# Optimization experiments

Hardware: AMD Instinct MI355X
Metric: run time of the kernel (lower is better)

## Reference

```python
import jax, jax.numpy as jnp
import numpy as np


def fwht(x):
    """Unnormalized fast Walsh-Hadamard transform over a 1-D vector (len = power of 2).
    Matches the torch chunk/cat stage ordering (MSB-first butterfly)."""
    n = x.shape[0]
    ll = int(round(np.log2(n)))
    for ii in range(ll):
        x = x.reshape(2 ** ii, 2, -1)
        x = jnp.concatenate([x[:, :1] + x[:, 1:], x[:, :1] - x[:, 1:]], axis=1)
    return x.reshape(n)


@jax.custom_vjp
def fwht_ff(x):
    # mirrors torch FastWalshHadamard.apply: plain FWHT forward,
    # backward = FWHT(grad) / sqrt(n) (as defined in the original autograd Function)
    return fwht(x)

def _fwht_ff_fwd(x):
    scale = jnp.asarray(1.0 / np.sqrt(float(x.shape[0])), x.dtype)
    return fwht(x), scale

def _fwht_ff_bwd(scale, g):
    return (scale * fwht(g),)

fwht_ff.defvjp(_fwht_ff_fwd, _fwht_ff_bwd)


def fastfood(theta, BB, Pi, GG, DD):
    """Fastfood projection of theta (dim dd) to DD dims using fixed vars."""
    LL = BB.shape[0]
    dd = theta.shape[0]
    k = min(dd, LL)  # F.pad with negative pad truncates; replicate that
    xx = jnp.zeros(LL, theta.dtype).at[:k].set(theta[:k])
    m2 = fwht(BB * xx)          # H B x
    m4 = m2[Pi] * GG            # G Pi H B x
    m5 = fwht_ff(m4)            # H G Pi H B x
    divisor = jnp.sqrt(LL * jnp.sum(GG * GG))
    return m5[:DD] / (divisor * np.sqrt(float(DD) / LL))


def _mk_ff_vars(key, DD):
    ll = int(np.ceil(np.log2(DD)))
    LL = 2 ** ll
    k1, k2, k3 = jax.random.split(key, 3)
    BB = jax.random.randint(k1, (LL,), 0, 2).astype(jnp.float32) * 2.0 - 1.0
    Pi = jax.random.permutation(k2, LL).astype(jnp.int32)
    GG = jax.random.normal(k3, (LL,), dtype=jnp.float32)
    return BB, Pi, GG


D_IN, D_HID, D_OUT = 768, 3072, 768
INTRINSIC = 2048
BATCH = 256


def setup_inputs() -> dict:
    key = jax.random.key(0)
    ks = jax.random.split(key, 12)
    x = jax.random.normal(ks[0], (BATCH, D_IN), dtype=jnp.float32)
    # original initializes intrinsic_parameter to zeros; use small randn so the
    # Fastfood path contributes non-trivially to the output for testing
    theta = jax.random.normal(ks[1], (INTRINSIC,), dtype=jnp.float32) * 0.01
    init_W1 = jax.random.normal(ks[2], (D_HID, D_IN), dtype=jnp.float32) * 0.02
    init_b1 = jax.random.normal(ks[3], (D_HID,), dtype=jnp.float32) * 0.02
    init_W2 = jax.random.normal(ks[4], (D_OUT, D_HID), dtype=jnp.float32) * 0.02
    init_b2 = jax.random.normal(ks[5], (D_OUT,), dtype=jnp.float32) * 0.02
    BB_W1, Pi_W1, GG_W1 = _mk_ff_vars(ks[6], D_HID * D_IN)
    BB_b1, Pi_b1, GG_b1 = _mk_ff_vars(ks[7], D_HID)
    BB_W2, Pi_W2, GG_W2 = _mk_ff_vars(ks[8], D_OUT * D_HID)
    BB_b2, Pi_b2, GG_b2 = _mk_ff_vars(ks[9], D_OUT)
    return {
        'x': x, 'theta': theta,
        'init_W1': init_W1, 'init_b1': init_b1, 'init_W2': init_W2, 'init_b2': init_b2,
        'BB_W1': BB_W1, 'Pi_W1': Pi_W1, 'GG_W1': GG_W1,
        'BB_b1': BB_b1, 'Pi_b1': Pi_b1, 'GG_b1': GG_b1,
        'BB_W2': BB_W2, 'Pi_W2': Pi_W2, 'GG_W2': GG_W2,
        'BB_b2': BB_b2, 'Pi_b2': Pi_b2, 'GG_b2': GG_b2,
    }


def reference(x, theta, init_W1, init_b1, init_W2, init_b2,
              BB_W1, Pi_W1, GG_W1, BB_b1, Pi_b1, GG_b1,
              BB_W2, Pi_W2, GG_W2, BB_b2, Pi_b2, GG_b2):
    # param = initial_value + fastfood(theta) for every wrapped parameter
    W1 = init_W1 + fastfood(theta, BB_W1, Pi_W1, GG_W1, init_W1.size).reshape(init_W1.shape)
    b1 = init_b1 + fastfood(theta, BB_b1, Pi_b1, GG_b1, init_b1.size)
    W2 = init_W2 + fastfood(theta, BB_W2, Pi_W2, GG_W2, init_W2.size).reshape(init_W2.shape)
    b2 = init_b2 + fastfood(theta, BB_b2, Pi_b2, GG_b2, init_b2.size)
    # wrapped module forward: Linear -> ReLU -> Linear
    h = jax.nn.relu(x @ W1.T + b1)
    return h @ W2.T + b2
```

## Files before the change

### kernel.cpp

```cpp
#include <hip/hip_runtime.h>
#include <hip/hip_bf16.h>

typedef __attribute__((ext_vector_type(8))) short bf16x8;
typedef __attribute__((ext_vector_type(8))) unsigned short u16x8;
typedef __attribute__((ext_vector_type(4))) float f32x4;

template <int N, int S>
__device__ __forceinline__ void reg_fwht(float* v) {
#pragma unroll
  for (int h = 1; h < N; h <<= 1)
#pragma unroll
    for (int g = 0; g < N; g += 2 * h)
#pragma unroll
      for (int j = 0; j < h; ++j) {
        float a = v[(g + j) * S], b = v[(g + j + h) * S];
        v[(g + j) * S] = a + b;
        v[(g + j + h) * S] = a - b;
      }
}

__device__ __forceinline__ unsigned short f2bf(float f) {
  unsigned u = __float_as_uint(f);
  unsigned r = (u + 0x7fff + ((u >> 16) & 1)) >> 16;
  return (unsigned short)r;
}

__device__ __forceinline__ void lds_fwht(float* s, int n, int tid, int T) {
  for (int h = 1; h < n; h <<= 1) {
    __syncthreads();
    for (int t = tid; t < (n >> 1); t += T) {
      int i0 = ((t & ~(h - 1)) << 1) | (t & (h - 1));
      int i1 = i0 + h;
      float a = s[i0], b = s[i1];
      s[i0] = a + b;
      s[i1] = a - b;
    }
  }
  __syncthreads();
}

__device__ __forceinline__ void fwht2048_block(float w[8], float* pad,
                                               float* dst, int t) {
  reg_fwht<8, 1>(w);
#pragma unroll
  for (int j = 0; j < 8; ++j) {
    int i = t + 256 * j;
    pad[i + 4 * (i >> 5)] = w[j];
  }
  __syncthreads();
  {
    int base = 8 * t + 4 * (t >> 2);
    float4 a = *(float4*)(pad + base);
    float4 b = *(float4*)(pad + base + 4);
    float u[8] = {a.x, a.y, a.z, a.w, b.x, b.y, b.z, b.w};
    reg_fwht<8, 1>(u);
    *(float4*)(pad + base) = make_float4(u[0], u[1], u[2], u[3]);
    *(float4*)(pad + base + 4) = make_float4(u[4], u[5], u[6], u[7]);
  }
  __syncthreads();
  {
    int b0 = (t & 7) + 64 * (t >> 3);
    float u[8];
#pragma unroll
    for (int j = 0; j < 8; ++j) {
      int i = b0 + 8 * j;
      u[j] = pad[i + 4 * (i >> 5)];
    }
    reg_fwht<8, 1>(u);
#pragma unroll
    for (int j = 0; j < 8; ++j) {
      int i = b0 + 8 * j;
      pad[i + 4 * (i >> 5)] = u[j];
    }
  }
  __syncthreads();
#pragma unroll
  for (int g = 0; g < 2; ++g) {
    int b0 = (t & 63) + 256 * ((g << 2) | (t >> 6));
    float u[4];
#pragma unroll
    for (int j = 0; j < 4; ++j) {
      int i = b0 + 64 * j;
      u[j] = pad[i + 4 * (i >> 5)];
    }
    reg_fwht<4, 1>(u);
#pragma unroll
    for (int j = 0; j < 4; ++j) dst[b0 + 64 * j] = u[j];
  }
  __syncthreads();
}

#define LLW 4194304

__global__ __launch_bounds__(256) void k_front(
    const float* __restrict__ BB1, const int* __restrict__ Pi1,
    const float* __restrict__ GG1, const float* __restrict__ BB2,
    const int* __restrict__ Pi2, const float* __restrict__ GG2,
    unsigned short* __restrict__ m4b, float* __restrict__ partial,
    const float* __restrict__ theta, const float* __restrict__ BBb1,
    const int* __restrict__ Pib1, const float* __restrict__ GGb1,
    const float* __restrict__ ib1, float* __restrict__ b1w,
    const float* __restrict__ BBb2, const int* __restrict__ Pib2,
    const float* __restrict__ GGb2, const float* __restrict__ ib2,
    float* __restrict__ b2w, const float* __restrict__ x,
    __hip_bfloat16* __restrict__ xb) {
  __shared__ __align__(16) float s[9216];
  __shared__ float red[4];
  int b = blockIdx.x, t = threadIdx.x;

  if (b < 1024) {
    int pipe = b >> 9, chunk = b & 511;
    const float* BB = pipe ? BB2 : BB1;
    const int* Pi = pipe ? Pi2 : Pi1;
    const float* GG = pipe ? GG2 : GG1;

    {
      float w8[8];
#pragma unroll
      for (int j = 0; j < 8; ++j) {
        int i = t + 256 * j;
        w8[j] = BB[i] * theta[i];
      }
      fwht2048_block(w8, s + 2304, s, t);
    }

    long base = (long)chunk * 8192;
    const int4* p4 = (const int4*)(Pi + base);
    const float4* g4 = (const float4*)(GG + base);
    float v[32];
    float lsum = 0.f;
#pragma unroll
    for (int j = 0; j < 8; ++j) {
      int4 p = p4[t + j * 256];
      float4 g = g4[t + j * 256];
      lsum += g.x * g.x + g.y * g.y + g.z * g.z + g.w * g.w;
      v[j * 4 + 0] = s[p.x & 2047] * g.x;
      v[j * 4 + 1] = s[p.y & 2047] * g.y;
      v[j * 4 + 2] = s[p.z & 2047] * g.z;
      v[j * 4 + 3] = s[p.w & 2047] * g.w;
    }
    for (int off = 32; off; off >>= 1) lsum += __shfl_down(lsum, off, 64);
    if ((t & 63) == 0) red[t >> 6] = lsum;

#pragma unroll
    for (int e = 0; e < 4; ++e) reg_fwht<8, 4>(v + e);

    __syncthreads();
    if (t == 0) partial[pipe * 512 + chunk] = red[0] + red[1] + red[2] + red[3];

#pragma unroll
    for (int j = 0; j < 8; ++j) {
      int A = t * 4 + 4 * (t >> 3) + j * 1152;
      *(float4*)(s + A) =
          make_float4(v[j * 4], v[j * 4 + 1], v[j * 4 + 2], v[j * 4 + 3]);
    }
    __syncthreads();
    {
      int b0 = (t & 31) + (t >> 5) * 1024;
      float w[32];
#pragma unroll
      for (int j2 = 0; j2 < 32; ++j2) {
        int i = b0 + j2 * 32;
        w[j2] = s[i + 4 * (i >> 5)];
      }
      reg_fwht<32, 1>(w);
#pragma unroll
      for (int j2 = 0; j2 < 32; ++j2) {
        int i = b0 + j2 * 32;
        s[i + 4 * (i >> 5)] = w[j2];
      }
    }
    __syncthreads();
#pragma unroll
    for (int q = 0; q < 8; ++q) {
      float4 r = *(const float4*)(s + t * 36 + q * 4);
      v[q * 4 + 0] = r.x;
      v[q * 4 + 1] = r.y;
      v[q * 4 + 2] = r.z;
      v[q * 4 + 3] = r.w;
    }
    reg_fwht<32, 1>(v);
    unsigned short* o = m4b + (long)pipe * LLW;
    long a0 = (long)(2 * t) * 8192 + (long)chunk * 16;
#pragma unroll
    for (int q = 0; q < 4; ++q) {
      u16x8 pk;
#pragma unroll
      for (int e = 0; e < 8; ++e) pk[e] = f2bf(v[q * 8 + e]);
      *(u16x8*)(o + a0 + (q >> 1) * 8192 + (q & 1) * 8) = pk;
    }
  } else if (b == 1024) {
    float* tabd = s + 6144;
    float w[8];
#pragma unroll
    for (int j = 0; j < 8; ++j) {
      int i = t + 256 * j;
      w[j] = BBb1[i] * theta[i];
    }
    fwht2048_block(w, s, tabd, t);

    float w16[16];
    float lsum = 0.f;
#pragma unroll
    for (int j = 0; j < 16; ++j) {
      int i = t + 256 * j;
      float g = GGb1[i];
      lsum += g * g;
      w16[j] = tabd[Pib1[i] & 2047] * g;
    }
    reg_fwht<16, 1>(w16);
#pragma unroll
    for (int j = 0; j < 16; ++j) {
      int i = t + 256 * j;
      s[i + 4 * (i >> 5)] = w16[j];
    }
    for (int off = 32; off; off >>= 1) lsum += __shfl_down(lsum, off, 64);
    if ((t & 63) == 0) s[4608 + (t >> 6)] = lsum;
    __syncthreads();
    float S = s[4608] + s[4609] + s[4610] + s[4611];
    {
      int base16 = 16 * t + 4 * (t >> 1);
      float u[16];
#pragma unroll
      for (int q = 0; q < 4; ++q) {
        float4 r = *(float4*)(s + base16 + q * 4);
        u[q * 4 + 0] = r.x;
        u[q * 4 + 1] = r.y;
        u[q * 4 + 2] = r.z;
        u[q * 4 + 3] = r.w;
      }
      reg_fwht<16, 1>(u);
#pragma unroll
      for (int q = 0; q < 4; ++q)
        *(float4*)(s + base16 + q * 4) =
            make_float4(u[q * 4], u[q * 4 + 1], u[q * 4 + 2], u[q * 4 + 3]);
    }
    __syncthreads();
    {
      float scale = 1.0f / sqrtf(S * 3072.0f);
      int b0 = (t & 15) + 256 * (t >> 4);
      float u[16];
#pragma unroll
      for (int j = 0; j < 16; ++j) {
        int i = b0 + 16 * j;
        u[j] = s[i + 4 * (i >> 5)];
      }
      reg_fwht<16, 1>(u);
#pragma unroll
      for (int j = 0; j < 16; ++j) {
        int i = b0 + 16 * j;
        if (i < 3072) b1w[i] = ib1[i] + u[j] * scale;
      }
    }
  } else if (b == 1025) {
    float* tab2 = s;
    float* m42 = s + 1024;
    for (int i = t; i < 1024; i += 256) tab2[i] = BBb2[i] * theta[i];
    lds_fwht(tab2, 1024, t, 256);
    float lsum = 0.f;
    for (int i = t; i < 1024; i += 256) {
      float g = GGb2[i];
      lsum += g * g;
      m42[i] = tab2[Pib2[i] & 1023] * g;
    }
    for (int off = 32; off; off >>= 1) lsum += __shfl_down(lsum, off, 64);
    if ((t & 63) == 0) s[2048 + (t >> 6)] = lsum;
    lds_fwht(m42, 1024, t, 256);
    float S = s[2048] + s[2049] + s[2050] + s[2051];
    float scale = 1.0f / sqrtf(S * 768.0f);
    for (int i = t; i < 768; i += 256) b2w[i] = ib2[i] + m42[i] * scale;
  } else {
    int id0 = (b - 1026) * 256 + t;
#pragma unroll
    for (int it = 0; it < 2; ++it) {
      int id = id0 + it * 24576;
      float4 xv = ((const float4*)x)[id];
      ushort4 o;
      o.x = f2bf(xv.x);
      o.y = f2bf(xv.y);
      o.z = f2bf(xv.z);
      o.w = f2bf(xv.w);
      ((ushort4*)xb)[id] = o;
    }
  }
}

__device__ __forceinline__ void f2c_body(const unsigned short* __restrict__ mpipe,
                                         const float* __restrict__ initW,
                                         unsigned short* __restrict__ outW,
                                         const float* __restrict__ partial_p,
                                         int lb, int t, float* s, float* red) {
  int g = ((lb & 7) << 6) | (lb >> 3);
  int l0 = g * 16;
  const unsigned short* mp = mpipe + (long)g * 8192;

  {
    float ps = partial_p[t] + partial_p[256 + t];
    for (int off = 32; off; off >>= 1) ps += __shfl_down(ps, off, 64);
    if ((t & 63) == 0) red[t >> 6] = ps;
  }

#pragma unroll
  for (int q = 0; q < 4; ++q) {
    u16x8 raw = *(const u16x8*)(mp + t * 32 + q * 8);
    int r = 2 * t + (q >> 1), cb = (q & 1) * 8;
    float* dp = s + r * 20 + (r >> 5) * 16 + cb;
    float4 f0, f1v;
    f0.x = __uint_as_float((unsigned)raw[0] << 16);
    f0.y = __uint_as_float((unsigned)raw[1] << 16);
    f0.z = __uint_as_float((unsigned)raw[2] << 16);
    f0.w = __uint_as_float((unsigned)raw[3] << 16);
    f1v.x = __uint_as_float((unsigned)raw[4] << 16);
    f1v.y = __uint_as_float((unsigned)raw[5] << 16);
    f1v.z = __uint_as_float((unsigned)raw[6] << 16);
    f1v.w = __uint_as_float((unsigned)raw[7] << 16);
    *(float4*)dp = f0;
    *(float4*)(dp + 4) = f1v;
  }
  __syncthreads();

  {
    int c = t & 15, rg = t >> 4;
    float w[32];
#pragma unroll
    for (int j = 0; j < 32; ++j) {
      int r = rg * 32 + j;
      w[j] = s[r * 20 + (r >> 5) * 16 + c];
    }
    reg_fwht<32, 1>(w);
#pragma unroll
    for (int j = 0; j < 32; ++j) {
      int r = rg * 32 + j;
      s[r * 20 + (r >> 5) * 16 + c] = w[j];
    }
  }
  __syncthreads();

  {
    int c = t & 15;
    float w[32];
#pragma unroll
    for (int k = 0; k < 2; ++k) {
      int b0 = (t >> 4) * 2 + k;
#pragma unroll
      for (int j4 = 0; j4 < 16; ++j4) {
        int r = b0 + 32 * j4;
        w[k * 16 + j4] = s[r * 20 + (r >> 5) * 16 + c];
      }
      reg_fwht<16, 1>(w + k * 16);
#pragma unroll
      for (int j4 = 0; j4 < 16; ++j4) {
        int r = b0 + 32 * j4;
        s[r * 20 + (r >> 5) * 16 + c] = w[k * 16 + j4];
      }
    }
  }
  __syncthreads();

  float S = red[0] + red[1] + red[2] + red[3];
  float scale = 1.0f / sqrtf(S * 2359296.0f);
#pragma unroll
  for (int u = 0; u < 5; ++u) {
    int idx = t + u * 256;
    if (idx < 1152) {
      int r = idx >> 2, c4 = (idx & 3) * 4;
      const float* sp = s + r * 20 + (r >> 5) * 16 + c4;
      long gi = (long)r * 8192 + l0 + c4;
      float4 iv = *(const float4*)(initW + gi);
      ushort4 pk;
      pk.x = f2bf(iv.x + sp[0] * scale);
      pk.y = f2bf(iv.y + sp[1] * scale);
      pk.z = f2bf(iv.z + sp[2] * scale);
      pk.w = f2bf(iv.w + sp[3] * scale);
      *(ushort4*)(outW + gi) = pk;
    }
  }
}

template <int NACC, int SPLITK, bool RELU, bool OUT_BF16>
__device__ __forceinline__ void gemm_body(
    const __hip_bfloat16* __restrict__ A, const __hip_bfloat16* __restrict__ B,
    const float* __restrict__ bias, void* __restrict__ C, int M, int N, int K,
    int bid, int tid, float* red) {
  int wave = tid >> 6, lane = tid & 63;
  int tileid = bid * (4 / SPLITK) + wave / SPLITK;
  int sk = wave % SPLITK;
  int ntiles = N / (16 * NACC);
  int mt = tileid / ntiles, nt = tileid % ntiles;
  int ml = lane & 15;
  int q = lane >> 4;
  const short* As = (const short*)A;
  const short* Bs = (const short*)B;
  long arow = (long)(mt * 16 + ml) * K + q * 8;
  int KS = K / SPLITK, k0 = sk * KS;
  f32x4 acc[NACC] = {};
  for (int k = k0; k < k0 + KS; k += 32) {
    bf16x8 av = *(const bf16x8*)(As + arow + k);
#pragma unroll
    for (int a = 0; a < NACC; ++a) {
      int n = nt * 16 * NACC + a * 16 + ml;
      bf16x8 bv = *(const bf16x8*)(Bs + (long)n * K + q * 8 + k);
      acc[a] = __builtin_amdgcn_mfma_f32_16x16x32_bf16(av, bv, acc[a], 0, 0, 0);
    }
  }
#pragma unroll
  for (int a = 0; a < NACC; ++a)
#pragma unroll
    for (int r = 0; r < 4; ++r)
      red[(wave * NACC + a) * 320 + lane * 5 + r] = acc[a][r];
  __syncthreads();
  if (sk == 0) {
#pragma unroll
    for (int a = 0; a < NACC; ++a) {
      int n = nt * 16 * NACC + a * 16 + ml;
      float bv = bias[n];
#pragma unroll
      for (int r = 0; r < 4; ++r) {
        float vv = bv;
#pragma unroll
        for (int j = 0; j < SPLITK; ++j)
          vv += red[((wave + j) * NACC + a) * 320 + lane * 5 + r];
        int mm = mt * 16 + q * 4 + r;
        if (RELU) vv = fmaxf(vv, 0.f);
        if (OUT_BF16)
          ((__hip_bfloat16*)C)[(long)mm * N + n] = __float2bfloat16(vv);
        else
          ((float*)C)[(long)mm * N + n] = vv;
      }
    }
  }
}

__global__ __launch_bounds__(256) void k_f2c_a(
    const unsigned short* __restrict__ m4b, const float* __restrict__ iW1,
    const float* __restrict__ partial, __hip_bfloat16* __restrict__ W1b) {
  __shared__ __align__(16) float s[10480];
  __shared__ float red[4];
  f2c_body(m4b, iW1, (unsigned short*)W1b, partial, blockIdx.x, threadIdx.x, s,
           red);
}

__global__ __launch_bounds__(256) void k_mix(
    const unsigned short* __restrict__ m4b, const float* __restrict__ iW2,
    const float* __restrict__ partial, __hip_bfloat16* __restrict__ W2b,
    const __hip_bfloat16* __restrict__ xb, const __hip_bfloat16* __restrict__ W1b,
    const float* __restrict__ b1w, __hip_bfloat16* __restrict__ hb) {
  __shared__ __align__(16) float s[10480];
  __shared__ float red[4];
  int b = blockIdx.x, t = threadIdx.x;
  if (b < 512) {
    f2c_body(m4b + (long)LLW, iW2, (unsigned short*)W2b, partial + 512, b, t,
             s, red);
  } else {
    gemm_body<2, 2, true, true>(xb, W1b, b1w, hb, 256, 3072, 768, b - 512, t,
                                s);
  }
}

template <int NACC, int SPLITK, bool RELU, bool OUT_BF16>
__global__ __launch_bounds__(256) void k_gemm(
    const __hip_bfloat16* __restrict__ A, const __hip_bfloat16* __restrict__ B,
    const float* __restrict__ bias, void* __restrict__ C, int M, int N, int K) {
  __shared__ float red[4 * NACC * 320];
  gemm_body<NACC, SPLITK, RELU, OUT_BF16>(A, B, bias, C, M, N, K, blockIdx.x,
                                          threadIdx.x, red);
}

#define OFF_PART 0
#define OFF_M2S 4096
#define OFF_M4B (OFF_M2S + 16384)
#define OFF_W1B (OFF_M4B + 2 * LLW * 2)
#define OFF_W2B (OFF_W1B + 4718592)
#define OFF_HB (OFF_W2B + 4718592)
#define OFF_XB (OFF_HB + 1572864)
#define OFF_B1 (OFF_XB + 393216)
#define OFF_B2 (OFF_B1 + 12288)

extern "C" void kernel_launch(void* const* d_in, const int* in_sizes, int n_in,
                              void* d_out, int out_size, void* d_ws,
                              size_t ws_size, hipStream_t stream) {
  const float* x = (const float*)d_in[0];
  const float* theta = (const float*)d_in[1];
  const float* iW1 = (const float*)d_in[2];
  const float* ib1 = (const float*)d_in[3];
  const float* iW2 = (const float*)d_in[4];
  const float* ib2 = (const float*)d_in[5];
  const float* BB_W1 = (const float*)d_in[6];
  const int* Pi_W1 = (const int*)d_in[7];
  const float* GG_W1 = (const float*)d_in[8];
  const float* BB_b1 = (const float*)d_in[9];
  const int* Pi_b1 = (const int*)d_in[10];
  const float* GG_b1 = (const float*)d_in[11];
  const float* BB_W2 = (const float*)d_in[12];
  const int* Pi_W2 = (const int*)d_in[13];
  const float* GG_W2 = (const float*)d_in[14];
  const float* BB_b2 = (const float*)d_in[15];
  const int* Pi_b2 = (const int*)d_in[16];
  const float* GG_b2 = (const float*)d_in[17];

  char* ws = (char*)d_ws;
  float* partial = (float*)(ws + OFF_PART);
  unsigned short* m4b = (unsigned short*)(ws + OFF_M4B);
  __hip_bfloat16* W1b = (__hip_bfloat16*)(ws + OFF_W1B);
  __hip_bfloat16* W2b = (__hip_bfloat16*)(ws + OFF_W2B);
  __hip_bfloat16* hb = (__hip_bfloat16*)(ws + OFF_HB);
  __hip_bfloat16* xb = (__hip_bfloat16*)(ws + OFF_XB);
  float* b1w = (float*)(ws + OFF_B1);
  float* b2w = (float*)(ws + OFF_B2);

  k_front<<<1122, 256, 0, stream>>>(BB_W1, Pi_W1, GG_W1, BB_W2, Pi_W2, GG_W2,
                                    m4b, partial, theta, BB_b1, Pi_b1, GG_b1,
                                    ib1, b1w, BB_b2, Pi_b2, GG_b2, ib2, b2w, x,
                                    xb);
  k_f2c_a<<<512, 256, 0, stream>>>(m4b, iW1, partial, W1b);
  k_mix<<<1280, 256, 0, stream>>>(m4b, iW2, partial, W2b, xb, W1b, b1w, hb);
  k_gemm<1, 4, false, false><<<768, 256, 0, stream>>>(hb, W2b, b2w, d_out, 256,
                                                      768, 3072);
}
```

Measured before the change: 218.1 us.

## Fuse all stages into one cooperative persistent kernel with grid syncs

Replaces the four separate launches with a single cooperative kernel of 1024 blocks that runs the front FWHT, the second FWHT/convert stage, GEMM1 and GEMM2, separated by grid-wide barriers. The small bias jobs and the x-to-bf16 conversion are folded into the front-stage blocks. The LDS padding in f2c is also removed so the kernel fits at four blocks per CU, and GEMM1 now uses three accumulators with 4-way split-K to cover 1024 blocks. The goal is to cut launch gaps and kernel tails, at the cost of grid-sync overhead and more bank conflicts from the unpadded LDS layout. If the cooperative launch fails, separate kernels run as a fallback.

```diff
diff --git a/kernel.cpp b/kernel.cpp
--- a/kernel.cpp
+++ b/kernel.cpp
@@ -1,9 +1,28 @@
 #include <hip/hip_runtime.h>
 #include <hip/hip_bf16.h>
+#include <hip/hip_cooperative_groups.h>
+
+namespace cg = cooperative_groups;
 
 typedef __attribute__((ext_vector_type(8))) short bf16x8;
 typedef __attribute__((ext_vector_type(8))) unsigned short u16x8;
 typedef __attribute__((ext_vector_type(4))) float f32x4;
+
+#define LLW 4194304
+
+struct FFParams {
+  const float* BB1; const int* Pi1; const float* GG1;
+  const float* BB2; const int* Pi2; const float* GG2;
+  unsigned short* m4b; float* partial; const float* theta;
+  const float* BBb1; const int* Pib1; const float* GGb1; const float* ib1;
+  float* b1w;
+  const float* BBb2; const int* Pib2; const float* GGb2; const float* ib2;
+  float* b2w;
+  const float* x; __hip_bfloat16* xb;
+  const float* iW1; const float* iW2;
+  __hip_bfloat16* W1b; __hip_bfloat16* W2b;
+  __hip_bfloat16* hb; float* out;
+};
 
 template <int N, int S>
 __device__ __forceinline__ void reg_fwht(float* v) {
@@ -90,206 +109,179 @@
   __syncthreads();
 }
 
-#define LLW 4194304
-
-__global__ __launch_bounds__(256) void k_front(
-    const float* __restrict__ BB1, const int* __restrict__ Pi1,
-    const float* __restrict__ GG1, const float* __restrict__ BB2,
-    const int* __restrict__ Pi2, const float* __restrict__ GG2,
-    unsigned short* __restrict__ m4b, float* __restrict__ partial,
-    const float* __restrict__ theta, const float* __restrict__ BBb1,
-    const int* __restrict__ Pib1, const float* __restrict__ GGb1,
-    const float* __restrict__ ib1, float* __restrict__ b1w,
-    const float* __restrict__ BBb2, const int* __restrict__ Pib2,
-    const float* __restrict__ GGb2, const float* __restrict__ ib2,
-    float* __restrict__ b2w, const float* __restrict__ x,
-    __hip_bfloat16* __restrict__ xb) {
-  __shared__ __align__(16) float s[9216];
-  __shared__ float red[4];
-  int b = blockIdx.x, t = threadIdx.x;
-
-  if (b < 1024) {
-    int pipe = b >> 9, chunk = b & 511;
-    const float* BB = pipe ? BB2 : BB1;
-    const int* Pi = pipe ? Pi2 : Pi1;
-    const float* GG = pipe ? GG2 : GG1;
-
-    {
-      float w8[8];
-#pragma unroll
-      for (int j = 0; j < 8; ++j) {
-        int i = t + 256 * j;
-        w8[j] = BB[i] * theta[i];
-      }
-      fwht2048_block(w8, s + 2304, s, t);
-    }
-
-    long base = (long)chunk * 8192;
-    const int4* p4 = (const int4*)(Pi + base);
-    const float4* g4 = (const float4*)(GG + base);
-    float v[32];
-    float lsum = 0.f;
-#pragma unroll
-    for (int j = 0; j < 8; ++j) {
-      int4 p = p4[t + j * 256];
-      float4 g = g4[t + j * 256];
-      lsum += g.x * g.x + g.y * g.y + g.z * g.z + g.w * g.w;
-      v[j * 4 + 0] = s[p.x & 2047] * g.x;
-      v[j * 4 + 1] = s[p.y & 2047] * g.y;
-      v[j * 4 + 2] = s[p.z & 2047] * g.z;
-      v[j * 4 + 3] = s[p.w & 2047] * g.w;
-    }
-    for (int off = 32; off; off >>= 1) lsum += __shfl_down(lsum, off, 64);
-    if ((t & 63) == 0) red[t >> 6] = lsum;
-
-#pragma unroll
-    for (int e = 0; e < 4; ++e) reg_fwht<8, 4>(v + e);
-
-    __syncthreads();
-    if (t == 0) partial[pipe * 512 + chunk] = red[0] + red[1] + red[2] + red[3];
-
-#pragma unroll
-    for (int j = 0; j < 8; ++j) {
-      int A = t * 4 + 4 * (t >> 3) + j * 1152;
-      *(float4*)(s + A) =
-          make_float4(v[j * 4], v[j * 4 + 1], v[j * 4 + 2], v[j * 4 + 3]);
-    }
-    __syncthreads();
-    {
-      int b0 = (t & 31) + (t >> 5) * 1024;
-      float w[32];
-#pragma unroll
-      for (int j2 = 0; j2 < 32; ++j2) {
-        int i = b0 + j2 * 32;
-        w[j2] = s[i + 4 * (i >> 5)];
-      }
-      reg_fwht<32, 1>(w);
-#pragma unroll
-      for (int j2 = 0; j2 < 32; ++j2) {
-        int i = b0 + j2 * 32;
-        s[i + 4 * (i >> 5)] = w[j2];
-      }
-    }
-    __syncthreads();
-#pragma unroll
-    for (int q = 0; q < 8; ++q) {
-      float4 r = *(const float4*)(s + t * 36 + q * 4);
-      v[q * 4 + 0] = r.x;
-      v[q * 4 + 1] = r.y;
-      v[q * 4 + 2] = r.z;
-      v[q * 4 + 3] = r.w;
-    }
-    reg_fwht<32, 1>(v);
-    unsigned short* o = m4b + (long)pipe * LLW;
-    long a0 = (long)(2 * t) * 8192 + (long)chunk * 16;
-#pragma unroll
-    for (int q = 0; q < 4; ++q) {
-      u16x8 pk;
-#pragma unroll
-      for (int e = 0; e < 8; ++e) pk[e] = f2bf(v[q * 8 + e]);
-      *(u16x8*)(o + a0 + (q >> 1) * 8192 + (q & 1) * 8) = pk;
-    }
-  } else if (b == 1024) {
-    float* tabd = s + 6144;
-    float w[8];
+__device__ __forceinline__ void front_pipe(const FFParams& p, int b, int t,
+                                           float* s, float* red) {
+  int pipe = b >> 9, chunk = b & 511;
+  const float* BB = pipe ? p.BB2 : p.BB1;
+  const int* Pi = pipe ? p.Pi2 : p.Pi1;
+  const float* GG = pipe ? p.GG2 : p.GG1;
+
+  {
+    float w8[8];
 #pragma unroll
     for (int j = 0; j < 8; ++j) {
       int i = t + 256 * j;
-      w[j] = BBb1[i] * theta[i];
-    }
-    fwht2048_block(w, s, tabd, t);
-
-    float w16[16];
-    float lsum = 0.f;
+      w8[j] = BB[i] * p.theta[i];
+    }
+    fwht2048_block(w8, s + 2304, s, t);
+  }
+
+  long base = (long)chunk * 8192;
+  const int4* p4 = (const int4*)(Pi + base);
+  const float4* g4 = (const float4*)(GG + base);
+  float v[32];
+  float lsum = 0.f;
+#pragma unroll
+  for (int j = 0; j < 8; ++j) {
+    int4 pp = p4[t + j * 256];
+    float4 g = g4[t + j * 256];
+    lsum += g.x * g.x + g.y * g.y + g.z * g.z + g.w * g.w;
+    v[j * 4 + 0] = s[pp.x & 2047] * g.x;
+    v[j * 4 + 1] = s[pp.y & 2047] * g.y;
+    v[j * 4 + 2] = s[pp.z & 2047] * g.z;
+    v[j * 4 + 3] = s[pp.w & 2047] * g.w;
+  }
+  for (int off = 32; off; off >>= 1) lsum += __shfl_down(lsum, off, 64);
+  if ((t & 63) == 0) red[t >> 6] = lsum;
+
+#pragma unroll
+  for (int e = 0; e < 4; ++e) reg_fwht<8, 4>(v + e);
+
+  __syncthreads();
+  if (t == 0)
+    p.partial[pipe * 512 + chunk] = red[0] + red[1] + red[2] + red[3];
+
+#pragma unroll
+  for (int j = 0; j < 8; ++j) {
+    int A = t * 4 + 4 * (t >> 3) + j * 1152;
+    *(float4*)(s + A) =
+        make_float4(v[j * 4], v[j * 4 + 1], v[j * 4 + 2], v[j * 4 + 3]);
+  }
+  __syncthreads();
+  {
+    int b0 = (t & 31) + (t >> 5) * 1024;
+    float w[32];
+#pragma unroll
+    for (int j2 = 0; j2 < 32; ++j2) {
+      int i = b0 + j2 * 32;
+      w[j2] = s[i + 4 * (i >> 5)];
+    }
+    reg_fwht<32, 1>(w);
+#pragma unroll
+    for (int j2 = 0; j2 < 32; ++j2) {
+      int i = b0 + j2 * 32;
+      s[i + 4 * (i >> 5)] = w[j2];
+    }
+  }
+  __syncthreads();
+#pragma unroll
+  for (int q = 0; q < 8; ++q) {
+    float4 r = *(const float4*)(s + t * 36 + q * 4);
+    v[q * 4 + 0] = r.x;
+    v[q * 4 + 1] = r.y;
+    v[q * 4 + 2] = r.z;
+    v[q * 4 + 3] = r.w;
+  }
+  reg_fwht<32, 1>(v);
+  unsigned short* o = p.m4b + (long)pipe * LLW;
+  long a0 = (long)(2 * t) * 8192 + (long)chunk * 16;
+#pragma unroll
+  for (int q = 0; q < 4; ++q) {
+    u16x8 pk;
+#pragma unroll
+    for (int e = 0; e < 8; ++e) pk[e] = f2bf(v[q * 8 + e]);
+    *(u16x8*)(o + a0 + (q >> 1) * 8192 + (q & 1) * 8) = pk;
+  }
+}
+
+__device__ __forceinline__ void bias1_job(const FFParams& p, int t, float* s) {
+  float* tabd = s + 6144;
+  float w[8];
+#pragma unroll
+  for (int j = 0; j < 8; ++j) {
+    int i = t + 256 * j;
+    w[j] = p.BBb1[i] * p.theta[i];
+  }
+  fwht2048_block(w, s, tabd, t);
+
+  float w16[16];
+  float lsum = 0.f;
+#pragma unroll
+  for (int j = 0; j < 16; ++j) {
+    int i = t + 256 * j;
+    float g = p.GGb1[i];
+    lsum += g * g;
+    w16[j] = tabd[p.Pib1[i] & 2047] * g;
+  }
+  reg_fwht<16, 1>(w16);
+#pragma unroll
+  for (int j = 0; j < 16; ++j) {
+    int i = t + 256 * j;
+    s[i + 4 * (i >> 5)] = w16[j];
+  }
+  for (int off = 32; off; off >>= 1) lsum += __shfl_down(lsum, off, 64);
+  if ((t & 63) == 0) s[4608 + (t >> 6)] = lsum;
+  __syncthreads();
+  float S = s[4608] + s[4609] + s[4610] + s[4611];
+  {
+    int base16 = 16 * t + 4 * (t >> 1);
+    float u[16];
+#pragma unroll
+    for (int q = 0; q < 4; ++q) {
+      float4 r = *(float4*)(s + base16 + q * 4);
+      u[q * 4 + 0] = r.x;
+      u[q * 4 + 1] = r.y;
+      u[q * 4 + 2] = r.z;
+      u[q * 4 + 3] = r.w;
+    }
+    reg_fwht<16, 1>(u);
+#pragma unroll
+    for (int q = 0; q < 4; ++q)
+      *(float4*)(s + base16 + q * 4) =
+          make_float4(u[q * 4], u[q * 4 + 1], u[q * 4 + 2], u[q * 4 + 3]);
+  }
+  __syncthreads();
+  {
+    float scale = 1.0f / sqrtf(S * 3072.0f);
+    int b0 = (t & 15) + 256 * (t >> 4);
+    float u[16];
 #pragma unroll
     for (int j = 0; j < 16; ++j) {
-      int i = t + 256 * j;
-      float g = GGb1[i];
-      lsum += g * g;
-      w16[j] = tabd[Pib1[i] & 2047] * g;
-    }
-    reg_fwht<16, 1>(w16);
+      int i = b0 + 16 * j;
+      u[j] = s[i + 4 * (i >> 5)];
+    }
+    reg_fwht<16, 1>(u);
 #pragma unroll
     for (int j = 0; j < 16; ++j) {
-      int i = t + 256 * j;
-      s[i + 4 * (i >> 5)] = w16[j];
-    }
-    for (int off = 32; off; off >>= 1) lsum += __shfl_down(lsum, off, 64);
-    if ((t & 63) == 0) s[4608 + (t >> 6)] = lsum;
-    __syncthreads();
-    float S = s[4608] + s[4609] + s[4610] + s[4611];
-    {
-      int base16 = 16 * t + 4 * (t >> 1);
-      float u[16];
-#pragma unroll
-      for (int q = 0; q < 4; ++q) {
-        float4 r = *(float4*)(s + base16 + q * 4);
-        u[q * 4 + 0] = r.x;
-        u[q * 4 + 1] = r.y;
-        u[q * 4 + 2] = r.z;
-        u[q * 4 + 3] = r.w;
-      }
-      reg_fwht<16, 1>(u);
-#pragma unroll
-      for (int q = 0; q < 4; ++q)
-        *(float4*)(s + base16 + q * 4) =
-            make_float4(u[q * 4], u[q * 4 + 1], u[q * 4 + 2], u[q * 4 + 3]);
-    }
-    __syncthreads();
-    {
-      float scale = 1.0f / sqrtf(S * 3072.0f);
-      int b0 = (t & 15) + 256 * (t >> 4);
-      float u[16];
-#pragma unroll
-      for (int j = 0; j < 16; ++j) {
-        int i = b0 + 16 * j;
-        u[j] = s[i + 4 * (i >> 5)];
-      }
-      reg_fwht<16, 1>(u);
-#pragma unroll
-      for (int j = 0; j < 16; ++j) {
-        int i = b0 + 16 * j;
-        if (i < 3072) b1w[i] = ib1[i] + u[j] * scale;
-      }
-    }
-  } else if (b == 1025) {
-    float* tab2 = s;
-    float* m42 = s + 1024;
-    for (int i = t; i < 1024; i += 256) tab2[i] = BBb2[i] * theta[i];
-    lds_fwht(tab2, 1024, t, 256);
-    float lsum = 0.f;
-    for (int i = t; i < 1024; i += 256) {
-      float g = GGb2[i];
-      lsum += g * g;
-      m42[i] = tab2[Pib2[i] & 1023] * g;
-    }
-    for (int off = 32; off; off >>= 1) lsum += __shfl_down(lsum, off, 64);
-    if ((t & 63) == 0) s[2048 + (t >> 6)] = lsum;
-    lds_fwht(m42, 1024, t, 256);
-    float S = s[2048] + s[2049] + s[2050] + s[2051];
-    float scale = 1.0f / sqrtf(S * 768.0f);
-    for (int i = t; i < 768; i += 256) b2w[i] = ib2[i] + m42[i] * scale;
-  } else {
-    int id0 = (b - 1026) * 256 + t;
-#pragma unroll
-    for (int it = 0; it < 2; ++it) {
-      int id = id0 + it * 24576;
-      float4 xv = ((const float4*)x)[id];
-      ushort4 o;
-      o.x = f2bf(xv.x);
-      o.y = f2bf(xv.y);
-      o.z = f2bf(xv.z);
-      o.w = f2bf(xv.w);
-      ((ushort4*)xb)[id] = o;
-    }
-  }
-}
-
-__device__ __forceinline__ void f2c_body(const unsigned short* __restrict__ mpipe,
-                                         const float* __restrict__ initW,
-                                         unsigned short* __restrict__ outW,
-                                         const float* __restrict__ partial_p,
-                                         int lb, int t, float* s, float* red) {
+      int i = b0 + 16 * j;
+      if (i < 3072) p.b1w[i] = p.ib1[i] + u[j] * scale;
+    }
+  }
+}
+
+__device__ __forceinline__ void bias2_job(const FFParams& p, int t, float* s) {
+  float* tab2 = s;
+  float* m42 = s + 1024;
+  for (int i = t; i < 1024; i += 256) tab2[i] = p.BBb2[i] * p.theta[i];
+  lds_fwht(tab2, 1024, t, 256);
+  float lsum = 0.f;
+  for (int i = t; i < 1024; i += 256) {
+    float g = p.GGb2[i];
+    lsum += g * g;
+    m42[i] = tab2[p.Pib2[i] & 1023] * g;
+  }
+  for (int off = 32; off; off >>= 1) lsum += __shfl_down(lsum, off, 64);
+  if ((t & 63) == 0) s[2048 + (t >> 6)] = lsum;
+  lds_fwht(m42, 1024, t, 256);
+  float S = s[2048] + s[2049] + s[2050] + s[2051];
+  float scale = 1.0f / sqrtf(S * 768.0f);
+  for (int i = t; i < 768; i += 256) p.b2w[i] = p.ib2[i] + m42[i] * scale;
+}
+
+__device__ __forceinline__ void f2c_body(
+    const unsigned short* __restrict__ mpipe, const float* __restrict__ initW,
+    unsigned short* __restrict__ outW, const float* __restrict__ partial_p,
+    int lb, int t, float* s, float* red) {
   int g = ((lb & 7) << 6) | (lb >> 3);
   int l0 = g * 16;
   const unsigned short* mp = mpipe + (long)g * 8192;
@@ -304,7 +296,7 @@
   for (int q = 0; q < 4; ++q) {
     u16x8 raw = *(const u16x8*)(mp + t * 32 + q * 8);
     int r = 2 * t + (q >> 1), cb = (q & 1) * 8;
-    float* dp = s + r * 20 + (r >> 5) * 16 + cb;
+    float* dp = s + r * 20 + cb;
     float4 f0, f1v;
     f0.x = __uint_as_float((unsigned)raw[0] << 16);
     f0.y = __uint_as_float((unsigned)raw[1] << 16);
@@ -325,13 +317,13 @@
 #pragma unroll
     for (int j = 0; j < 32; ++j) {
       int r = rg * 32 + j;
-      w[j] = s[r * 20 + (r >> 5) * 16 + c];
+      w[j] = s[r * 20 + c];
     }
     reg_fwht<32, 1>(w);
 #pragma unroll
     for (int j = 0; j < 32; ++j) {
       int r = rg * 32 + j;
-      s[r * 20 + (r >> 5) * 16 + c] = w[j];
+      s[r * 20 + c] = w[j];
     }
   }
   __syncthreads();
@@ -345,13 +337,13 @@
 #pragma unroll
       for (int j4 = 0; j4 < 16; ++j4) {
         int r = b0 + 32 * j4;
-        w[k * 16 + j4] = s[r * 20 + (r >> 5) * 16 + c];
+        w[k * 16 + j4] = s[r * 20 + c];
       }
       reg_fwht<16, 1>(w + k * 16);
 #pragma unroll
       for (int j4 = 0; j4 < 16; ++j4) {
         int r = b0 + 32 * j4;
-        s[r * 20 + (r >> 5) * 16 + c] = w[k * 16 + j4];
+        s[r * 20 + c] = w[k * 16 + j4];
       }
     }
   }
@@ -364,7 +356,7 @@
     int idx = t + u * 256;
     if (idx < 1152) {
       int r = idx >> 2, c4 = (idx & 3) * 4;
-      const float* sp = s + r * 20 + (r >> 5) * 16 + c4;
+      const float* sp = s + r * 20 + c4;
       long gi = (long)r * 8192 + l0 + c4;
       float4 iv = *(const float4*)(initW + gi);
       ushort4 pk;
@@ -431,39 +423,97 @@
   }
 }
 
-__global__ __launch_bounds__(256) void k_f2c_a(
-    const unsigned short* __restrict__ m4b, const float* __restrict__ iW1,
-    const float* __restrict__ partial, __hip_bfloat16* __restrict__ W1b) {
-  __shared__ __align__(16) float s[10480];
-  __shared__ float red[4];
-  f2c_body(m4b, iW1, (unsigned short*)W1b, partial, blockIdx.x, threadIdx.x, s,
-           red);
-}
-
-__global__ __launch_bounds__(256) void k_mix(
-    const unsigned short* __restrict__ m4b, const float* __restrict__ iW2,
-    const float* __restrict__ partial, __hip_bfloat16* __restrict__ W2b,
-    const __hip_bfloat16* __restrict__ xb, const __hip_bfloat16* __restrict__ W1b,
-    const float* __restrict__ b1w, __hip_bfloat16* __restrict__ hb) {
-  __shared__ __align__(16) float s[10480];
-  __shared__ float red[4];
+__global__ __launch_bounds__(256, 4) void k_mega(FFParams p) {
+  __shared__ __align__(16) float s[10240];
+  float* red = s + 10236;
   int b = blockIdx.x, t = threadIdx.x;
-  if (b < 512) {
-    f2c_body(m4b + (long)LLW, iW2, (unsigned short*)W2b, partial + 512, b, t,
-             s, red);
+
+  if (t < 48) {
+    int id = b * 48 + t;
+    float4 xv = ((const float4*)p.x)[id];
+    ushort4 o;
+    o.x = f2bf(xv.x);
+    o.y = f2bf(xv.y);
+    o.z = f2bf(xv.z);
+    o.w = f2bf(xv.w);
+    ((ushort4*)p.xb)[id] = o;
+  }
+  front_pipe(p, b, t, s, red);
+  if (b == 0) {
+    __syncthreads();
+    bias1_job(p, t, s);
+  } else if (b == 1) {
+    __syncthreads();
+    bias2_job(p, t, s);
+  }
+
+  cg::this_grid().sync();
+
+  {
+    int pipe = b >> 9, lb = b & 511;
+    f2c_body(p.m4b + (long)pipe * LLW, pipe ? p.iW2 : p.iW1,
+             (unsigned short*)(pipe ? p.W2b : p.W1b), p.partial + pipe * 512,
+             lb, t, s, red);
+  }
+
+  cg::this_grid().sync();
+
+  gemm_body<3, 4, true, true>(p.xb, p.W1b, p.b1w, p.hb, 256, 3072, 768, b, t,
+                              s);
+
+  cg::this_grid().sync();
+
+  if (b < 768)
+    gemm_body<1, 4, false, false>(p.hb, p.W2b, p.b2w, p.out, 256, 768, 3072, b,
+                                  t, s);
+}
+
+__global__ __launch_bounds__(256) void k_front_sa(FFParams p) {
+  __shared__ __align__(16) float s[10240];
+  float* red = s + 10236;
+  int b = blockIdx.x, t = threadIdx.x;
+  if (b < 1024) {
+    front_pipe(p, b, t, s, red);
+  } else if (b == 1024) {
+    bias1_job(p, t, s);
+  } else if (b == 1025) {
+    bias2_job(p, t, s);
   } else {
-    gemm_body<2, 2, true, true>(xb, W1b, b1w, hb, 256, 3072, 768, b - 512, t,
-                                s);
-  }
-}
-
-template <int NACC, int SPLITK, bool RELU, bool OUT_BF16>
-__global__ __launch_bounds__(256) void k_gemm(
-    const __hip_bfloat16* __restrict__ A, const __hip_bfloat16* __restrict__ B,
-    const float* __restrict__ bias, void* __restrict__ C, int M, int N, int K) {
-  __shared__ float red[4 * NACC * 320];
-  gemm_body<NACC, SPLITK, RELU, OUT_BF16>(A, B, bias, C, M, N, K, blockIdx.x,
-                                          threadIdx.x, red);
+    int id0 = (b - 1026) * 256 + t;
+#pragma unroll
+    for (int it = 0; it < 2; ++it) {
+      int id = id0 + it * 24576;
+      float4 xv = ((const float4*)p.x)[id];
+      ushort4 o;
+      o.x = f2bf(xv.x);
+      o.y = f2bf(xv.y);
+      o.z = f2bf(xv.z);
+      o.w = f2bf(xv.w);
+      ((ushort4*)p.xb)[id] = o;
+    }
+  }
+}
+
+__global__ __launch_bounds__(256) void k_f2c_sa(FFParams p) {
+  __shared__ __align__(16) float s[10240];
+  float* red = s + 10236;
+  int b = blockIdx.x, t = threadIdx.x;
+  int pipe = b >> 9, lb = b & 511;
+  f2c_body(p.m4b + (long)pipe * LLW, pipe ? p.iW2 : p.iW1,
+           (unsigned short*)(pipe ? p.W2b : p.W1b), p.partial + pipe * 512, lb,
+           t, s, red);
+}
+
+__global__ __launch_bounds__(256) void k_gemm1_sa(FFParams p) {
+  __shared__ __align__(16) float s[2560];
+  gemm_body<2, 2, true, true>(p.xb, p.W1b, p.b1w, p.hb, 256, 3072, 768,
+                              blockIdx.x, threadIdx.x, s);
+}
+
+__global__ __launch_bounds__(256) void k_gemm2_sa(FFParams p) {
+  __shared__ __align__(16) float s[1280];
+  gemm_body<1, 4, false, false>(p.hb, p.W2b, p.b2w, p.out, 256, 768, 3072,
+                                blockIdx.x, threadIdx.x, s);
 }
 
 #define OFF_PART 0
@@ -479,41 +529,44 @@
 extern "C" void kernel_launch(void* const* d_in, const int* in_sizes, int n_in,
                               void* d_out, int out_size, void* d_ws,
                               size_t ws_size, hipStream_t stream) {
-  const float* x = (const float*)d_in[0];
-  const float* theta = (const float*)d_in[1];
-  const float* iW1 = (const float*)d_in[2];
-  const float* ib1 = (const float*)d_in[3];
-  const float* iW2 = (const float*)d_in[4];
-  const float* ib2 = (const float*)d_in[5];
-  const float* BB_W1 = (const float*)d_in[6];
-  const int* Pi_W1 = (const int*)d_in[7];
-  const float* GG_W1 = (const float*)d_in[8];
-  const float* BB_b1 = (const float*)d_in[9];
-  const int* Pi_b1 = (const int*)d_in[10];
-  const float* GG_b1 = (const float*)d_in[11];
-  const float* BB_W2 = (const float*)d_in[12];
-  const int* Pi_W2 = (const int*)d_in[13];
-  const float* GG_W2 = (const float*)d_in[14];
-  const float* BB_b2 = (const float*)d_in[15];
-  const int* Pi_b2 = (const int*)d_in[16];
-  const float* GG_b2 = (const float*)d_in[17];
-
   char* ws = (char*)d_ws;
-  float* partial = (float*)(ws + OFF_PART);
-  unsigned short* m4b = (unsigned short*)(ws + OFF_M4B);
-  __hip_bfloat16* W1b = (__hip_bfloat16*)(ws + OFF_W1B);
-  __hip_bfloat16* W2b = (__hip_bfloat16*)(ws + OFF_W2B);
-  __hip_bfloat16* hb = (__hip_bfloat16*)(ws + OFF_HB);
-  __hip_bfloat16* xb = (__hip_bfloat16*)(ws + OFF_XB);
-  float* b1w = (float*)(ws + OFF_B1);
-  float* b2w = (float*)(ws + OFF_B2);
-
-  k_front<<<1122, 256, 0, stream>>>(BB_W1, Pi_W1, GG_W1, BB_W2, Pi_W2, GG_W2,
-                                    m4b, partial, theta, BB_b1, Pi_b1, GG_b1,
-                                    ib1, b1w, BB_b2, Pi_b2, GG_b2, ib2, b2w, x,
-                                    xb);
-  k_f2c_a<<<512, 256, 0, stream>>>(m4b, iW1, partial, W1b);
-  k_mix<<<1280, 256, 0, stream>>>(m4b, iW2, partial, W2b, xb, W1b, b1w, hb);
-  k_gemm<1, 4, false, false><<<768, 256, 0, stream>>>(hb, W2b, b2w, d_out, 256,
-                                                      768, 3072);
-}
+  FFParams p;
+  p.x = (const float*)d_in[0];
+  p.theta = (const float*)d_in[1];
+  p.iW1 = (const float*)d_in[2];
+  p.ib1 = (const float*)d_in[3];
+  p.iW2 = (const float*)d_in[4];
+  p.ib2 = (const float*)d_in[5];
+  p.BB1 = (const float*)d_in[6];
+  p.Pi1 = (const int*)d_in[7];
+  p.GG1 = (const float*)d_in[8];
+  p.BBb1 = (const float*)d_in[9];
+  p.Pib1 = (const int*)d_in[10];
+  p.GGb1 = (const float*)d_in[11];
+  p.BB2 = (const float*)d_in[12];
+  p.Pi2 = (const int*)d_in[13];
+  p.GG2 = (const float*)d_in[14];
+  p.BBb2 = (const float*)d_in[15];
+  p.Pib2 = (const int*)d_in[16];
+  p.GGb2 = (const float*)d_in[17];
+  p.partial = (float*)(ws + OFF_PART);
+  p.m4b = (unsigned short*)(ws + OFF_M4B);
+  p.W1b = (__hip_bfloat16*)(ws + OFF_W1B);
+  p.W2b = (__hip_bfloat16*)(ws + OFF_W2B);
+  p.hb = (__hip_bfloat16*)(ws + OFF_HB);
+  p.xb = (__hip_bfloat16*)(ws + OFF_XB);
+  p.b1w = (float*)(ws + OFF_B1);
+  p.b2w = (float*)(ws + OFF_B2);
+  p.out = (float*)d_out;
+
+  void* kargs[] = {(void*)&p};
+  hipError_t e = hipLaunchCooperativeKernel((const void*)k_mega, dim3(1024),
+                                            dim3(256), kargs, 0, stream);
+  if (e != hipSuccess) {
+    (void)hipGetLastError();
+    k_front_sa<<<1122, 256, 0, stream>>>(p);
+    k_f2c_sa<<<1024, 256, 0, stream>>>(p);
+    k_gemm1_sa<<<768, 256, 0, stream>>>(p);
+    k_gemm2_sa<<<768, 256, 0, stream>>>(p);
+  }
+}
```

Measured after the change: 621.7 us. 2.85x slower.
